# Performance work log

Measured on AMD Instinct MI355X. Metric: run time of the kernel, lower is better.

The kernel has to match this reference:

```python
import jax, jax.numpy as jnp
import numpy as np

N_NODES = 100000


def setup_inputs() -> dict:
    key = jax.random.key(0)
    ks = jax.random.split(key, 8)
    IN, HID, OUT = 128, 128, 64
    E = 1600000
    x = jax.random.normal(ks[0], (N_NODES, IN), dtype=jnp.float32)
    edge_index = jax.random.randint(ks[1], (2, E), 0, N_NODES, dtype=jnp.int64)
    # PyG SAGEConv params: lin_l (applied to aggregated neighbors, with bias),
    # lin_r (root weight, no bias).
    def lin(k, fi, fo):
        return jax.random.normal(k, (fi, fo), dtype=jnp.float32) / np.sqrt(fi)
    Wl0 = lin(ks[2], IN, HID)
    bl0 = jnp.zeros((HID,), dtype=jnp.float32)
    Wr0 = lin(ks[3], IN, HID)
    Wl1 = lin(ks[4], HID, OUT)
    bl1 = jnp.zeros((OUT,), dtype=jnp.float32)
    Wr1 = lin(ks[5], HID, OUT)
    return {"x": x, "edge_index": edge_index,
            "Wl0": Wl0, "bl0": bl0, "Wr0": Wr0,
            "Wl1": Wl1, "bl1": bl1, "Wr1": Wr1}


def _sage_conv(h, src, dst, Wl, bl, Wr):
    # mean aggregation of source features onto target nodes
    summed = jax.ops.segment_sum(h[src], dst, num_segments=N_NODES)  # [N, d]
    cnt = jax.ops.segment_sum(jnp.ones((src.shape[0], 1), h.dtype), dst,
                              num_segments=N_NODES)                  # [N, 1]
    agg = summed / jnp.maximum(cnt, 1.0)
    return agg @ Wl + bl + h @ Wr


def reference(x, edge_index, Wl0, bl0, Wr0, Wl1, bl1, Wr1):
    src, dst = edge_index[0], edge_index[1]
    h = jax.nn.relu(_sage_conv(x, src, dst, Wl0, bl0, Wr0))
    # dropout is identity in eval mode (training=False)
    return _sage_conv(h, src, dst, Wl1, bl1, Wr1)
```

## Files before the change

### kernel.cpp

```cpp
#include <hip/hip_runtime.h>


typedef short short8 __attribute__((ext_vector_type(8)));
typedef float f32x4 __attribute__((ext_vector_type(4)));
typedef float f32x2 __attribute__((ext_vector_type(2)));

#define NBUCK 782
#define BCAP  3072
#define EPB   8192

static __device__ __forceinline__ unsigned short f2bf(float f) {
    union { float f; unsigned u; } c; c.f = f;
    unsigned u = c.u + 0x7fffu + ((c.u >> 16) & 1u);
    return (unsigned short)(u >> 16);
}
static __device__ __forceinline__ float bf2f(unsigned short b) {
    union { unsigned u; float f; } c; c.u = ((unsigned)b) << 16;
    return c.f;
}
static __device__ __forceinline__ float bf2f_s(short b) {
    return bf2f((unsigned short)b);
}

static __device__ __forceinline__ unsigned char f2fp8(float x) {
    union { float f; unsigned u; } c; c.f = x;
    unsigned s = (c.u >> 24) & 0x80u;
    float a = __builtin_fabsf(x);
    if (a < 0.015625f) {
        int m = (int)rintf(a * 512.0f);
        return (unsigned char)(s | (unsigned)m);
    }
    unsigned u = c.u + 0x7ffffu + ((c.u >> 20) & 1u);
    int e = (int)((u >> 23) & 0xff) - 120;
    unsigned m = (u >> 20) & 7u;
    if (e > 15) { e = 15; m = 6; }
    return (unsigned char)(s | (unsigned)(e << 3) | m);
}

static __device__ __forceinline__ void acc_fp8x4(unsigned w, float* a) {
#if __has_builtin(__builtin_amdgcn_cvt_pk_f32_fp8)
    f32x2 lo = __builtin_amdgcn_cvt_pk_f32_fp8((int)w, false);
    f32x2 hi = __builtin_amdgcn_cvt_pk_f32_fp8((int)w, true);
    a[0] += lo[0]; a[1] += lo[1]; a[2] += hi[0]; a[3] += hi[1];
#else
    #pragma unroll
    for (int j = 0; j < 4; ++j) {
        unsigned b = (w >> (8 * j)) & 0xffu;
        union { unsigned u; float f; } c;
        c.u = ((b & 0x80u) << 24) | ((b & 0x7fu) << 20);
        a[j] += c.f * 0x1p120f;
    }
#endif
}
static __device__ __forceinline__ void acc_row16(uint4 w, float* a) {
    acc_fp8x4(w.x, a + 0);  acc_fp8x4(w.y, a + 4);
    acc_fp8x4(w.z, a + 8);  acc_fp8x4(w.w, a + 12);
}

__global__ __launch_bounds__(256) void k_pack(const float* __restrict__ WA,
                                              const float* __restrict__ WB,
                                              int CA, int NC,
                                              unsigned short* __restrict__ Wp) {
    int tid = blockIdx.x * 256 + threadIdx.x;
    if (tid >= NC * 16) return;
    int lane = tid & 63, kk = (tid >> 6) & 3, tg = tid >> 8;
    int l15 = lane & 15, quad = lane >> 4;
    int c = tg * 16 + l15;
    const float* W = (c < CA) ? WA : WB;
    int cc = (c < CA) ? c : c - CA;
    short8 v;
    #pragma unroll
    for (int j = 0; j < 8; ++j) {
        int k = kk * 32 + quad * 8 + j;
        v[j] = (short)f2bf(W[(size_t)k * CA + cc]);
    }
    *(short8*)(Wp + (size_t)tid * 8) = v;
}

__global__ __launch_bounds__(256) void k_gemm0_bucket(
        const float* __restrict__ X, const unsigned short* __restrict__ Wp,
        unsigned char* __restrict__ P0, unsigned short* __restrict__ Q0, int Nrows,
        const int* __restrict__ src, const int* __restrict__ dst,
        int* __restrict__ cursor, int* __restrict__ bregion,
        int E, int gemmBlocks) {
    const int t = threadIdx.x;
    if ((int)blockIdx.x < gemmBlocks) {
        const int wave = t >> 6, lane = t & 63;
        const int quad = lane >> 4, l15 = lane & 15;
        const int row0 = blockIdx.x * 32;
        const int c0w = wave * 64;
        f32x4 acc[2][4];
        #pragma unroll
        for (int mt = 0; mt < 2; ++mt)
            #pragma unroll
            for (int tt = 0; tt < 4; ++tt) acc[mt][tt] = (f32x4){0.f, 0.f, 0.f, 0.f};
        #pragma unroll
        for (int kk = 0; kk < 4; ++kk) {
            const int k0 = kk * 32 + quad * 8;
            short8 a[2];
            #pragma unroll
            for (int mt = 0; mt < 2; ++mt) {
                int row = row0 + mt * 16 + l15;
                if (row > Nrows - 1) row = Nrows - 1;
                const float* xp = X + (size_t)row * 128 + k0;
                float4 f0 = *(const float4*)xp;
                float4 f1 = *(const float4*)(xp + 4);
                short8 v;
                v[0] = (short)f2bf(f0.x); v[1] = (short)f2bf(f0.y);
                v[2] = (short)f2bf(f0.z); v[3] = (short)f2bf(f0.w);
                v[4] = (short)f2bf(f1.x); v[5] = (short)f2bf(f1.y);
                v[6] = (short)f2bf(f1.z); v[7] = (short)f2bf(f1.w);
                a[mt] = v;
            }
            short8 b[4];
            #pragma unroll
            for (int tt = 0; tt < 4; ++tt) {
                int tg = (c0w >> 4) + tt;
                b[tt] = *(const short8*)(Wp + ((size_t)(tg * 4 + kk) * 64 + lane) * 8);
            }
            #pragma unroll
            for (int mt = 0; mt < 2; ++mt)
                #pragma unroll
                for (int tt = 0; tt < 4; ++tt)
                    acc[mt][tt] = __builtin_amdgcn_mfma_f32_16x16x32_bf16(
                        a[mt], b[tt], acc[mt][tt], 0, 0, 0);
        }
        #pragma unroll
        for (int mt = 0; mt < 2; ++mt)
            #pragma unroll
            for (int r = 0; r < 4; ++r) {
                int row = row0 + mt * 16 + quad * 4 + r;
                if (row < Nrows) {
                    if (c0w < 128) {
                        #pragma unroll
                        for (int tt = 0; tt < 4; ++tt)
                            P0[(size_t)row * 128 + c0w + tt * 16 + l15] =
                                f2fp8(acc[mt][tt][r]);
                    } else {
                        #pragma unroll
                        for (int tt = 0; tt < 4; ++tt)
                            Q0[(size_t)row * 128 + (c0w - 128) + tt * 16 + l15] =
                                f2bf(acc[mt][tt][r]);
                    }
                }
            }
        return;
    }
    __shared__ int hist[NBUCK];
    __shared__ int basel[NBUCK];
    int bid = blockIdx.x - gemmBlocks;
    for (int i = t; i < NBUCK; i += 256) hist[i] = 0;
    __syncthreads();
    int e0 = bid * EPB + t * 32;
    int d[32];
    if (e0 + 32 <= E) {
        #pragma unroll
        for (int q = 0; q < 8; ++q) {
            int4 v = *(const int4*)(dst + e0 + q * 4);
            d[q * 4 + 0] = v.x; d[q * 4 + 1] = v.y;
            d[q * 4 + 2] = v.z; d[q * 4 + 3] = v.w;
        }
    } else {
        #pragma unroll
        for (int j = 0; j < 32; ++j) d[j] = (e0 + j < E) ? dst[e0 + j] : -1;
    }
    #pragma unroll
    for (int j = 0; j < 32; ++j)
        if (d[j] >= 0) atomicAdd(&hist[d[j] >> 7], 1);
    __syncthreads();
    for (int i = t; i < NBUCK; i += 256) {
        int c = hist[i];
        basel[i] = (c > 0) ? atomicAdd(&cursor[i], c) : 0;
    }
    __syncthreads();
    for (int i = t; i < NBUCK; i += 256) hist[i] = 0;
    __syncthreads();
    int s[32];
    if (e0 + 32 <= E) {
        #pragma unroll
        for (int q = 0; q < 8; ++q) {
            int4 v = *(const int4*)(src + e0 + q * 4);
            s[q * 4 + 0] = v.x; s[q * 4 + 1] = v.y;
            s[q * 4 + 2] = v.z; s[q * 4 + 3] = v.w;
        }
    } else {
        #pragma unroll
        for (int j = 0; j < 32; ++j) s[j] = (e0 + j < E) ? src[e0 + j] : 0;
    }
    #pragma unroll
    for (int j = 0; j < 32; ++j) {
        if (d[j] < 0) continue;
        int b = d[j] >> 7;
        int r = atomicAdd(&hist[b], 1);
        bregion[(size_t)b * BCAP + basel[b] + r] = s[j] | ((d[j] & 127) << 20);
    }
}

__global__ __launch_bounds__(256) void k_csr(const int* __restrict__ cursor,
                                             const int* __restrict__ bregion,
                                             int* __restrict__ rowptr,
                                             int* __restrict__ csr, int Nn) {
    __shared__ int words[BCAP];
    __shared__ int hist[128], sc[128], rank[128];
    __shared__ int red[256];
    int b = blockIdx.x, t = threadIdx.x;
    int part = 0;
    for (int i = t; i < b; i += 256) part += cursor[i];
    red[t] = part;
    if (t < 128) { hist[t] = 0; rank[t] = 0; }
    __syncthreads();
    #pragma unroll
    for (int off = 128; off > 0; off >>= 1) {
        if (t < off) red[t] += red[t + off];
        __syncthreads();
    }
    int gbase = red[0];
    int cnt = cursor[b];
    for (int i = t; i < cnt; i += 256) {
        int w = bregion[(size_t)b * BCAP + i];
        words[i] = w;
        atomicAdd(&hist[w >> 20], 1);
    }
    __syncthreads();
    if (t < 128) sc[t] = hist[t];
    __syncthreads();
    #pragma unroll
    for (int off = 1; off < 128; off <<= 1) {
        int x = 0;
        if (t < 128 && t >= off) x = sc[t - off];
        __syncthreads();
        if (t < 128) sc[t] += x;
        __syncthreads();
    }
    if (t < 128) sc[t] -= hist[t];
    __syncthreads();
    if (t < 128) {
        int node = b * 128 + t;
        if (node <= Nn) rowptr[node] = gbase + sc[t];
    }
    for (int i = t; i < cnt; i += 256) {
        int w = words[i];
        int d7 = w >> 20;
        int r = atomicAdd(&rank[d7], 1);
        csr[gbase + sc[d7] + r] = w & 0xFFFFF;
    }
}

__global__ __launch_bounds__(256) void k_gemm1(const unsigned short* __restrict__ Xv,
                                               const unsigned short* __restrict__ Wp,
                                               unsigned char* __restrict__ P1,
                                               unsigned short* __restrict__ Q1,
                                               int Nrows) {
    const int t = threadIdx.x;
    const int wave = t >> 6, lane = t & 63;
    const int quad = lane >> 4, l15 = lane & 15;
    const int row0 = blockIdx.x * 32;
    const int c0w = wave * 32;
    f32x4 acc[2][2];
    #pragma unroll
    for (int mt = 0; mt < 2; ++mt)
        #pragma unroll
        for (int tt = 0; tt < 2; ++tt) acc[mt][tt] = (f32x4){0.f, 0.f, 0.f, 0.f};
    #pragma unroll
    for (int kk = 0; kk < 4; ++kk) {
        const int k0 = kk * 32 + quad * 8;
        short8 a[2];
        #pragma unroll
        for (int mt = 0; mt < 2; ++mt) {
            int row = row0 + mt * 16 + l15;
            if (row > Nrows - 1) row = Nrows - 1;
            a[mt] = *(const short8*)(Xv + (size_t)row * 128 + k0);
        }
        short8 b[2];
        #pragma unroll
        for (int tt = 0; tt < 2; ++tt) {
            int tg = (c0w >> 4) + tt;
            b[tt] = *(const short8*)(Wp + ((size_t)(tg * 4 + kk) * 64 + lane) * 8);
        }
        #pragma unroll
        for (int mt = 0; mt < 2; ++mt)
            #pragma unroll
            for (int tt = 0; tt < 2; ++tt)
                acc[mt][tt] = __builtin_amdgcn_mfma_f32_16x16x32_bf16(
                    a[mt], b[tt], acc[mt][tt], 0, 0, 0);
    }
    #pragma unroll
    for (int mt = 0; mt < 2; ++mt)
        #pragma unroll
        for (int r = 0; r < 4; ++r) {
            int row = row0 + mt * 16 + quad * 4 + r;
            if (row < Nrows) {
                if (c0w < 64) {
                    #pragma unroll
                    for (int tt = 0; tt < 2; ++tt)
                        P1[(size_t)row * 64 + c0w + tt * 16 + l15] =
                            f2fp8(acc[mt][tt][r]);
                } else {
                    #pragma unroll
                    for (int tt = 0; tt < 2; ++tt)
                        Q1[(size_t)row * 64 + (c0w - 64) + tt * 16 + l15] =
                            f2bf(acc[mt][tt][r]);
                }
            }
        }
}

__global__ __launch_bounds__(256) void k_agg0(const unsigned char* __restrict__ P0,
                                              const unsigned short* __restrict__ Q0,
                                              const int* __restrict__ rowptr,
                                              const int* __restrict__ csr,
                                              const float* __restrict__ bl0,
                                              unsigned short* __restrict__ h, int Nn) {
    int wave = threadIdx.x >> 6, lane = threadIdx.x & 63;
    int g = lane >> 3, l7 = lane & 7;
    int n = (blockIdx.x * 4 + wave) * 8 + g;
    bool live = (n < Nn);
    int st = 0, dg = 0;
    if (live) { st = rowptr[n]; dg = rowptr[n + 1] - st; }
    float acc[16] = {};
    int e = 0;
    for (; e + 2 <= dg; e += 2) {
        int s0 = csr[st + e];
        int s1 = csr[st + e + 1];
        uint4 w0 = *(const uint4*)(P0 + (size_t)s0 * 128 + l7 * 16);
        uint4 w1 = *(const uint4*)(P0 + (size_t)s1 * 128 + l7 * 16);
        acc_row16(w0, acc);
        acc_row16(w1, acc);
    }
    if (e < dg) {
        int s0 = csr[st + e];
        uint4 w0 = *(const uint4*)(P0 + (size_t)s0 * 128 + l7 * 16);
        acc_row16(w0, acc);
    }
    if (live) {
        float inv = 1.f / fmaxf((float)dg, 1.f);
        short8 q0 = *(const short8*)(Q0 + (size_t)n * 128 + l7 * 16);
        short8 q1 = *(const short8*)(Q0 + (size_t)n * 128 + l7 * 16 + 8);
        float bb[16];
        *(float4*)(bb + 0)  = *(const float4*)(bl0 + l7 * 16);
        *(float4*)(bb + 4)  = *(const float4*)(bl0 + l7 * 16 + 4);
        *(float4*)(bb + 8)  = *(const float4*)(bl0 + l7 * 16 + 8);
        *(float4*)(bb + 12) = *(const float4*)(bl0 + l7 * 16 + 12);
        short8 o0, o1;
        #pragma unroll
        for (int j = 0; j < 8; ++j)
            o0[j] = (short)f2bf(fmaxf(acc[j] * inv + bb[j] + bf2f_s(q0[j]), 0.f));
        #pragma unroll
        for (int j = 0; j < 8; ++j)
            o1[j] = (short)f2bf(fmaxf(acc[8 + j] * inv + bb[8 + j] + bf2f_s(q1[j]), 0.f));
        *(short8*)(h + (size_t)n * 128 + l7 * 16) = o0;
        *(short8*)(h + (size_t)n * 128 + l7 * 16 + 8) = o1;
    }
}

__global__ __launch_bounds__(256) void k_agg1(const unsigned char* __restrict__ P1,
                                              const unsigned short* __restrict__ Q1,
                                              const int* __restrict__ rowptr,
                                              const int* __restrict__ csr,
                                              const float* __restrict__ bl1,
                                              float* __restrict__ out, int Nn) {
    int wave = threadIdx.x >> 6, lane = threadIdx.x & 63;
    int g = lane >> 2, l3 = lane & 3;
    int n = (blockIdx.x * 4 + wave) * 16 + g;
    bool live = (n < Nn);
    int st = 0, dg = 0;
    if (live) { st = rowptr[n]; dg = rowptr[n + 1] - st; }
    float acc[16] = {};
    int e = 0;
    for (; e + 2 <= dg; e += 2) {
        int s0 = csr[st + e];
        int s1 = csr[st + e + 1];
        uint4 w0 = *(const uint4*)(P1 + (size_t)s0 * 64 + l3 * 16);
        uint4 w1 = *(const uint4*)(P1 + (size_t)s1 * 64 + l3 * 16);
        acc_row16(w0, acc);
        acc_row16(w1, acc);
    }
    if (e < dg) {
        int s0 = csr[st + e];
        uint4 w0 = *(const uint4*)(P1 + (size_t)s0 * 64 + l3 * 16);
        acc_row16(w0, acc);
    }
    if (live) {
        float inv = 1.f / fmaxf((float)dg, 1.f);
        short8 q0 = *(const short8*)(Q1 + (size_t)n * 64 + l3 * 16);
        short8 q1 = *(const short8*)(Q1 + (size_t)n * 64 + l3 * 16 + 8);
        float bb[16];
        *(float4*)(bb + 0)  = *(const float4*)(bl1 + l3 * 16);
        *(float4*)(bb + 4)  = *(const float4*)(bl1 + l3 * 16 + 4);
        *(float4*)(bb + 8)  = *(const float4*)(bl1 + l3 * 16 + 8);
        *(float4*)(bb + 12) = *(const float4*)(bl1 + l3 * 16 + 12);
        float4 o[4];
        #pragma unroll
        for (int j = 0; j < 8; ++j)
            ((float*)o)[j] = acc[j] * inv + bb[j] + bf2f_s(q0[j]);
        #pragma unroll
        for (int j = 0; j < 8; ++j)
            ((float*)o)[8 + j] = acc[8 + j] * inv + bb[8 + j] + bf2f_s(q1[j]);
        #pragma unroll
        for (int q = 0; q < 4; ++q)
            *(float4*)(out + (size_t)n * 64 + l3 * 16 + q * 4) = o[q];
    }
}

extern "C" void kernel_launch(void* const* d_in, const int* in_sizes, int n_in,
                              void* d_out, int out_size, void* d_ws, size_t ws_size,
                              hipStream_t stream) {
    const float* x   = (const float*)d_in[0];
    const int* eidx  = (const int*)d_in[1];
    const float* Wl0 = (const float*)d_in[2];
    const float* bl0 = (const float*)d_in[3];
    const float* Wr0 = (const float*)d_in[4];
    const float* Wl1 = (const float*)d_in[5];
    const float* bl1 = (const float*)d_in[6];
    const float* Wr1 = (const float*)d_in[7];
    float* out = (float*)d_out;

    const int N = in_sizes[0] / 128;
    const int E = in_sizes[1] / 2;
    const int* src = eidx;
    const int* dst = eidx + E;

    int* rowptr  = (int*)d_ws;
    int* cursor  = rowptr + (N + 4);
    int* bregion = cursor + 784;
    int* csr     = bregion + (size_t)NBUCK * BCAP;
    unsigned short* Wp0 = (unsigned short*)(csr + E);
    unsigned short* Wp1 = Wp0 + 32768;
    unsigned char*  P0  = (unsigned char*)(Wp1 + 16384);
    unsigned short* Q0  = (unsigned short*)(P0 + (size_t)N * 128);
    unsigned short* h   = Q0 + (size_t)N * 128;
    unsigned char*  P1  = (unsigned char*)(h + (size_t)N * 128);
    unsigned short* Q1  = (unsigned short*)(P1 + (size_t)N * 64);

    hipMemsetAsync(cursor, 0, NBUCK * sizeof(int), stream);

    k_pack<<<(256 * 16 + 255) / 256, 256, 0, stream>>>(Wl0, Wr0, 128, 256, Wp0);
    k_pack<<<(128 * 16 + 255) / 256, 256, 0, stream>>>(Wl1, Wr1, 64, 128, Wp1);

    int gemmBlocks = (N + 31) / 32;
    int nbb = (E + EPB - 1) / EPB;
    k_gemm0_bucket<<<gemmBlocks + nbb, 256, 0, stream>>>(
        x, Wp0, P0, Q0, N, src, dst, cursor, bregion, E, gemmBlocks);
    k_csr<<<NBUCK, 256, 0, stream>>>(cursor, bregion, rowptr, csr, N);

    k_agg0<<<(N + 31) / 32, 256, 0, stream>>>(P0, Q0, rowptr, csr, bl0, h, N);
    k_gemm1<<<(N + 31) / 32, 256, 0, stream>>>(h, Wp1, P1, Q1, N);
    k_agg1<<<(N + 63) / 64, 256, 0, stream>>>(P1, Q1, rowptr, csr, bl1, out, N);
}
```

Baseline: 293.3 us.

## Merge weight pack launches, schedule bucket blocks first, stream edges without register arrays

The two weight-pack kernels become one launch covering both layers. In the fused gemm/bucket kernel the edge-bucketing blocks now take the lowest block indices, so they are dispatched first and their long atomic-heavy work overlaps with the GEMM blocks. The bucketing path no longer keeps 32-element dst/src register arrays; it streams int4 loads straight into LDS atomics and re-reads dst in the second pass. This lowers register pressure and launch overhead, at the cost of reading dst from global memory twice.

```diff
diff --git a/kernel.cpp b/kernel.cpp
--- a/kernel.cpp
+++ b/kernel.cpp
@@ -57,12 +57,19 @@
     acc_fp8x4(w.z, a + 8);  acc_fp8x4(w.w, a + 12);
 }
 
-__global__ __launch_bounds__(256) void k_pack(const float* __restrict__ WA,
-                                              const float* __restrict__ WB,
-                                              int CA, int NC,
-                                              unsigned short* __restrict__ Wp) {
+__global__ __launch_bounds__(256) void k_pack2(const float* __restrict__ Wl0,
+        const float* __restrict__ Wr0, const float* __restrict__ Wl1,
+        const float* __restrict__ Wr1, unsigned short* __restrict__ Wp0,
+        unsigned short* __restrict__ Wp1) {
     int tid = blockIdx.x * 256 + threadIdx.x;
-    if (tid >= NC * 16) return;
+    const float *WA, *WB; int CA; unsigned short* Wp;
+    if (tid < 4096) {
+        WA = Wl0; WB = Wr0; CA = 128; Wp = Wp0;
+    } else {
+        tid -= 4096;
+        if (tid >= 2048) return;
+        WA = Wl1; WB = Wr1; CA = 64; Wp = Wp1;
+    }
     int lane = tid & 63, kk = (tid >> 6) & 3, tg = tid >> 8;
     int l15 = lane & 15, quad = lane >> 4;
     int c = tg * 16 + l15;
@@ -82,12 +89,12 @@
         unsigned char* __restrict__ P0, unsigned short* __restrict__ Q0, int Nrows,
         const int* __restrict__ src, const int* __restrict__ dst,
         int* __restrict__ cursor, int* __restrict__ bregion,
-        int E, int gemmBlocks) {
+        int E, int bucketBlocks) {
     const int t = threadIdx.x;
-    if ((int)blockIdx.x < gemmBlocks) {
+    if ((int)blockIdx.x >= bucketBlocks) {
         const int wave = t >> 6, lane = t & 63;
         const int quad = lane >> 4, l15 = lane & 15;
-        const int row0 = blockIdx.x * 32;
+        const int row0 = (blockIdx.x - bucketBlocks) * 32;
         const int c0w = wave * 64;
         f32x4 acc[2][4];
         #pragma unroll
@@ -148,25 +155,23 @@
     }
     __shared__ int hist[NBUCK];
     __shared__ int basel[NBUCK];
-    int bid = blockIdx.x - gemmBlocks;
+    int bid = blockIdx.x;
     for (int i = t; i < NBUCK; i += 256) hist[i] = 0;
     __syncthreads();
     int e0 = bid * EPB + t * 32;
-    int d[32];
     if (e0 + 32 <= E) {
         #pragma unroll
         for (int q = 0; q < 8; ++q) {
             int4 v = *(const int4*)(dst + e0 + q * 4);
-            d[q * 4 + 0] = v.x; d[q * 4 + 1] = v.y;
-            d[q * 4 + 2] = v.z; d[q * 4 + 3] = v.w;
+            atomicAdd(&hist[v.x >> 7], 1);
+            atomicAdd(&hist[v.y >> 7], 1);
+            atomicAdd(&hist[v.z >> 7], 1);
+            atomicAdd(&hist[v.w >> 7], 1);
         }
     } else {
-        #pragma unroll
-        for (int j = 0; j < 32; ++j) d[j] = (e0 + j < E) ? dst[e0 + j] : -1;
-    }
-    #pragma unroll
-    for (int j = 0; j < 32; ++j)
-        if (d[j] >= 0) atomicAdd(&hist[d[j] >> 7], 1);
+        for (int j = 0; j < 32; ++j)
+            if (e0 + j < E) atomicAdd(&hist[dst[e0 + j] >> 7], 1);
+    }
     __syncthreads();
     for (int i = t; i < NBUCK; i += 256) {
         int c = hist[i];
@@ -175,24 +180,29 @@
     __syncthreads();
     for (int i = t; i < NBUCK; i += 256) hist[i] = 0;
     __syncthreads();
-    int s[32];
     if (e0 + 32 <= E) {
         #pragma unroll
         for (int q = 0; q < 8; ++q) {
-            int4 v = *(const int4*)(src + e0 + q * 4);
-            s[q * 4 + 0] = v.x; s[q * 4 + 1] = v.y;
-            s[q * 4 + 2] = v.z; s[q * 4 + 3] = v.w;
+            int4 dv = *(const int4*)(dst + e0 + q * 4);
+            int4 sv = *(const int4*)(src + e0 + q * 4);
+            int dd[4] = {dv.x, dv.y, dv.z, dv.w};
+            int ss[4] = {sv.x, sv.y, sv.z, sv.w};
+            #pragma unroll
+            for (int j = 0; j < 4; ++j) {
+                int b = dd[j] >> 7;
+                int r = atomicAdd(&hist[b], 1);
+                bregion[(size_t)b * BCAP + basel[b] + r] = ss[j] | ((dd[j] & 127) << 20);
+            }
         }
     } else {
-        #pragma unroll
-        for (int j = 0; j < 32; ++j) s[j] = (e0 + j < E) ? src[e0 + j] : 0;
-    }
-    #pragma unroll
-    for (int j = 0; j < 32; ++j) {
-        if (d[j] < 0) continue;
-        int b = d[j] >> 7;
-        int r = atomicAdd(&hist[b], 1);
-        bregion[(size_t)b * BCAP + basel[b] + r] = s[j] | ((d[j] & 127) << 20);
+        for (int j = 0; j < 32; ++j) {
+            if (e0 + j < E) {
+                int dd = dst[e0 + j], ss = src[e0 + j];
+                int b = dd >> 7;
+                int r = atomicAdd(&hist[b], 1);
+                bregion[(size_t)b * BCAP + basel[b] + r] = ss | ((dd & 127) << 20);
+            }
+        }
     }
 }
 
@@ -434,13 +444,12 @@
 
     hipMemsetAsync(cursor, 0, NBUCK * sizeof(int), stream);
 
-    k_pack<<<(256 * 16 + 255) / 256, 256, 0, stream>>>(Wl0, Wr0, 128, 256, Wp0);
-    k_pack<<<(128 * 16 + 255) / 256, 256, 0, stream>>>(Wl1, Wr1, 64, 128, Wp1);
+    k_pack2<<<24, 256, 0, stream>>>(Wl0, Wr0, Wl1, Wr1, Wp0, Wp1);
 
     int gemmBlocks = (N + 31) / 32;
     int nbb = (E + EPB - 1) / EPB;
     k_gemm0_bucket<<<gemmBlocks + nbb, 256, 0, stream>>>(
-        x, Wp0, P0, Q0, N, src, dst, cursor, bregion, E, gemmBlocks);
+        x, Wp0, P0, Q0, N, src, dst, cursor, bregion, E, nbb);
     k_csr<<<NBUCK, 256, 0, stream>>>(cursor, bregion, rowptr, csr, N);
 
     k_agg0<<<(N + 31) / 32, 256, 0, stream>>>(P0, Q0, rowptr, csr, bl0, h, N);
```

After: 296.6 us. Within noise of the previous version (+1.1%).
